# Kernel tuning notes

Hardware: AMD Instinct MI355X
Metric: run time of the kernel (lower is better)

Reference implementation:

```python
import jax, jax.numpy as jnp
import numpy as np

HEADS = 4
DIM_HEAD = 32
GN_EPS = 1e-6  # flax GroupNorm default


def setup_inputs() -> dict:
    key = jax.random.key(0)
    ks = jax.random.split(key, 3)
    B, H, W, C = 32, 64, 64, 256
    hidden = HEADS * DIM_HEAD  # 128
    x = jax.random.normal(ks[0], (B, H, W, C), dtype=jnp.float32)
    w_qkv = jax.random.normal(ks[1], (C, 3 * hidden), dtype=jnp.float32) * 0.02
    w_out = jax.random.normal(ks[2], (hidden, C), dtype=jnp.float32) * 0.02
    b_out = jnp.zeros((C,), dtype=jnp.float32)
    gn_scale = jnp.ones((C,), dtype=jnp.float32)
    gn_bias = jnp.zeros((C,), dtype=jnp.float32)
    return {"x": x, "w_qkv": w_qkv, "w_out": w_out, "b_out": b_out,
            "gn_scale": gn_scale, "gn_bias": gn_bias}


def reference(x, w_qkv, w_out, b_out, gn_scale, gn_bias):
    # x: [B, H, W, C] (flax Conv is channel-last)
    scale = DIM_HEAD ** (-0.5)
    qkv = jnp.einsum('bhwc,cd->bhwd', x, w_qkv)          # 1x1 conv, no bias
    q, k, v = jnp.split(qkv, 3, axis=-1)                 # each [B, H, W, hidden]
    q = jax.nn.softmax(q, axis=-2) * scale               # softmax over W axis
    k = jax.nn.softmax(k, axis=-1)                       # softmax over hidden axis
    # einsum axes as in source: b d n h / b e n h -> b d e h (d,e = H; n = W; h = hidden)
    context = jnp.einsum('bdnh,benh->bdeh', k, v)        # [B, H, H, hidden]
    out = jnp.einsum('bdeh,bdnh->benh', context, q)      # [B, H, W, hidden]
    y = jnp.einsum('bhwc,cd->bhwd', out, w_out) + b_out  # 1x1 conv with bias
    # GroupNorm(num_groups=1): normalize over (H, W, C) per sample
    mean = jnp.mean(y, axis=(1, 2, 3), keepdims=True)
    var = jnp.var(y, axis=(1, 2, 3), keepdims=True)
    y = (y - mean) * jax.lax.rsqrt(var + GN_EPS)
    return y * gn_scale + gn_bias
```

## Files before the change

kernel.cpp:

```cpp
#include <hip/hip_runtime.h>
#include <hip/hip_bf16.h>

typedef __hip_bfloat16 bf16;
typedef float f32x4 __attribute__((ext_vector_type(4)));
typedef short bf16x8 __attribute__((ext_vector_type(8)));
typedef short s16x4 __attribute__((ext_vector_type(4)));

#define NB 32
#define NC 256
#define NHID 128
#define NQKV 384
#define SMSCALE 0.17677669529663687f
#define PADA 264

__device__ __forceinline__ short f2bf(float f) {
  union { float f; unsigned u; } v;
  v.f = f;
  return (short)((v.u + 0x7fffu + ((v.u >> 16) & 1u)) >> 16);
}
__device__ __forceinline__ float bf2f(short s) {
  union { unsigned u; float f; } v;
  v.u = ((unsigned)(unsigned short)s) << 16;
  return v.f;
}

__global__ __launch_bounds__(256) void k_prep_w(const float* __restrict__ wqkv,
                                                const float* __restrict__ wout,
                                                short* __restrict__ wqt,
                                                short* __restrict__ wot) {
  int i = blockIdx.x * 256 + threadIdx.x;
  if (i < 98304) {
    int e = i & 7, l = (i >> 3) & 63, f = i >> 9;
    int nj = f % 6, g = f / 6;
    int ks = g & 7, s = g >> 3;
    int n = s * 96 + nj * 16 + (l & 15);
    int k = ks * 32 + (l >> 4) * 8 + e;
    wqt[i] = f2bf(wqkv[(size_t)k * NQKV + n]);
  }
  if (i < 32768) {
    int e = i & 7, l = (i >> 3) & 63, f = i >> 9;
    int nj = f & 3, g = f >> 2;
    int ks = g & 3, w = g >> 2;
    int c = w * 64 + nj * 16 + (l & 15);
    int k = ks * 32 + (l >> 4) * 8 + e;
    wot[i] = f2bf(wout[(size_t)k * NC + c]);
  }
}

__global__ __launch_bounds__(512) void k_gemm_qkv(const float* __restrict__ x,
                                                  const short* __restrict__ wqt,
                                                  short* __restrict__ qt,
                                                  short* __restrict__ kt,
                                                  short* __restrict__ vt) {
  __shared__ short As[64 * PADA];
  float* Ks = (float*)As;

  const int t = threadIdx.x;
  const int lane = t & 63;
  const int w = t >> 6;
  const int l15 = lane & 15;
  const int q = lane >> 4;
  const int h = w >> 2;
  const int strip = (w & 3) * 96;
  const int rowBase = blockIdx.x * 64;
  const int b = rowBase >> 12;
  const int d = (rowBase >> 6) & 63;

  {
    const int r = w;
    const int c = (t & 63) * 4;
#pragma unroll
    for (int it = 0; it < 8; ++it) {
      int row = it * 8 + r;
      float4 f = *(const float4*)(x + (size_t)(rowBase + row) * NC + c);
      s16x4 sv;
      sv[0] = f2bf(f.x); sv[1] = f2bf(f.y); sv[2] = f2bf(f.z); sv[3] = f2bf(f.w);
      *(s16x4*)(As + row * PADA + c) = sv;
    }
  }
  __syncthreads();

  const short* wqb = wqt + (((size_t)(w & 3) * 8) * 6) * 512 + lane * 8;

  f32x4 acc[2][6] = {};
  for (int ks = 0; ks < 8; ++ks) {
    const int k0 = ks * 32 + q * 8;
    bf16x8 afr[2];
#pragma unroll
    for (int mi = 0; mi < 2; ++mi)
      afr[mi] = *(const bf16x8*)(As + (h * 32 + mi * 16 + l15) * PADA + k0);
#pragma unroll
    for (int nj = 0; nj < 6; ++nj) {
      bf16x8 bfr = *(const bf16x8*)(wqb + (ks * 6 + nj) * 512);
#pragma unroll
      for (int mi = 0; mi < 2; ++mi)
        acc[mi][nj] = __builtin_amdgcn_mfma_f32_16x16x32_bf16(afr[mi], bfr, acc[mi][nj], 0, 0, 0);
    }
  }
  __syncthreads();

#pragma unroll
  for (int mi = 0; mi < 2; ++mi) {
#pragma unroll
    for (int nj = 0; nj < 6; ++nj) {
      const int g = strip + nj * 16 + l15;
      const int n_sp = h * 32 + mi * 16 + q * 4;
      if (g < 128) {
        s16x4 sv;
        sv[0] = f2bf(acc[mi][nj][0]); sv[1] = f2bf(acc[mi][nj][1]);
        sv[2] = f2bf(acc[mi][nj][2]); sv[3] = f2bf(acc[mi][nj][3]);
        *(s16x4*)(qt + (((size_t)(b * 128 + g)) << 12) + (d << 6) + n_sp) = sv;
      } else if (g < 256) {
        const int kc = g - 128;
#pragma unroll
        for (int rg = 0; rg < 4; ++rg)
          Ks[(n_sp + rg) * 132 + kc] = acc[mi][nj][rg];
      } else {
        s16x4 sv;
        sv[0] = f2bf(acc[mi][nj][0]); sv[1] = f2bf(acc[mi][nj][1]);
        sv[2] = f2bf(acc[mi][nj][2]); sv[3] = f2bf(acc[mi][nj][3]);
        *(s16x4*)(vt + (((size_t)(b * 128 + (g - 256))) << 12) + (d << 6) + n_sp) = sv;
      }
    }
  }
  __syncthreads();

  {
    const int r = t >> 3;
    const int c0 = (t & 7) * 16;
    float vals[16];
    float m = -1e30f;
#pragma unroll
    for (int i = 0; i < 16; ++i) {
      vals[i] = Ks[r * 132 + c0 + i];
      m = fmaxf(m, vals[i]);
    }
    m = fmaxf(m, __shfl_xor(m, 1, 64));
    m = fmaxf(m, __shfl_xor(m, 2, 64));
    m = fmaxf(m, __shfl_xor(m, 4, 64));
    float s = 0.f;
#pragma unroll
    for (int i = 0; i < 16; ++i) {
      vals[i] = __expf(vals[i] - m);
      s += vals[i];
    }
    s += __shfl_xor(s, 1, 64);
    s += __shfl_xor(s, 2, 64);
    s += __shfl_xor(s, 4, 64);
    const float rinv = 1.f / s;
#pragma unroll
    for (int i = 0; i < 16; ++i)
      Ks[r * 132 + c0 + i] = vals[i] * rinv;
  }
  __syncthreads();

  {
    const int n = t & 63;
    const int c0 = (t >> 6) * 16;
    const size_t obase = (((size_t)(b * 128)) << 12) + (d << 6) + n;
#pragma unroll
    for (int i = 0; i < 16; ++i)
      kt[obase + (((size_t)(c0 + i)) << 12)] = f2bf(Ks[n * 132 + c0 + i]);
  }
}

__global__ __launch_bounds__(256) void k_attn(const short* __restrict__ kt,
                                              const short* __restrict__ vt,
                                              const short* __restrict__ qt,
                                              short* __restrict__ at) {
  __shared__ short SK[4096];
  __shared__ short SV[4096];
  __shared__ short SC[4096];
  __shared__ short SP[4096];
  const int ch = blockIdx.x;
  const int b = blockIdx.y;
  const int t = threadIdx.x;
  const int lane = t & 63;
  const int w = t >> 6;
  const int l15 = lane & 15;
  const int q = lane >> 4;
  const size_t base = ((size_t)(b * 128 + ch)) << 12;

  {
    const int row = t >> 2;
    const int u0 = (t & 3) * 2;
    const int src = row * 64 + u0 * 8;
    bf16x8 k0 = *(const bf16x8*)(kt + base + src);
    bf16x8 k1 = *(const bf16x8*)(kt + base + src + 8);
    bf16x8 v0 = *(const bf16x8*)(vt + base + src);
    bf16x8 v1 = *(const bf16x8*)(vt + base + src + 8);
    const int r7 = row & 7;
    *(bf16x8*)(SK + row * 64 + ((u0 ^ r7) << 3)) = k0;
    *(bf16x8*)(SK + row * 64 + (((u0 + 1) ^ r7) << 3)) = k1;
    *(bf16x8*)(SV + row * 64 + ((u0 ^ r7) << 3)) = v0;
    *(bf16x8*)(SV + row * 64 + (((u0 + 1) ^ r7) << 3)) = v1;
  }
  {
    const int dd = t >> 2;
    const int c0 = (t & 3) * 16;
    bf16x8 q0 = *(const bf16x8*)(qt + base + dd * 64 + c0);
    bf16x8 q1 = *(const bf16x8*)(qt + base + dd * 64 + c0 + 8);
    float vals[16];
#pragma unroll
    for (int i = 0; i < 8; ++i) { vals[i] = bf2f(q0[i]); vals[8 + i] = bf2f(q1[i]); }
    float m = -1e30f;
#pragma unroll
    for (int i = 0; i < 16; ++i) m = fmaxf(m, vals[i]);
    m = fmaxf(m, __shfl_xor(m, 1, 64));
    m = fmaxf(m, __shfl_xor(m, 2, 64));
    float s = 0.f;
#pragma unroll
    for (int i = 0; i < 16; ++i) {
      vals[i] = __expf(vals[i] - m);
      s += vals[i];
    }
    s += __shfl_xor(s, 1, 64);
    s += __shfl_xor(s, 2, 64);
    const float r = SMSCALE / s;
    const int du = dd >> 3, doff = dd & 7;
#pragma unroll
    for (int i = 0; i < 16; ++i) {
      const int n = c0 + i;
      SP[n * 64 + ((du ^ (n & 7)) << 3) + doff] = f2bf(vals[i] * r);
    }
  }
  __syncthreads();

  f32x4 acc[4] = {};
#pragma unroll
  for (int ks = 0; ks < 2; ++ks) {
    const int rA = w * 16 + l15;
    bf16x8 afr = *(const bf16x8*)(SK + rA * 64 + (((ks * 4 + q) ^ (rA & 7)) << 3));
#pragma unroll
    for (int nj = 0; nj < 4; ++nj) {
      const int rB = nj * 16 + l15;
      bf16x8 bfr = *(const bf16x8*)(SV + rB * 64 + (((ks * 4 + q) ^ (rB & 7)) << 3));
      acc[nj] = __builtin_amdgcn_mfma_f32_16x16x32_bf16(afr, bfr, acc[nj], 0, 0, 0);
    }
  }
#pragma unroll
  for (int nj = 0; nj < 4; ++nj) {
    const int e = nj * 16 + l15;
    const int d0 = w * 16 + q * 4;
    s16x4 sv;
    sv[0] = f2bf(acc[nj][0]); sv[1] = f2bf(acc[nj][1]);
    sv[2] = f2bf(acc[nj][2]); sv[3] = f2bf(acc[nj][3]);
    *(s16x4*)(SC + e * 64 + (((d0 >> 3) ^ (e & 7)) << 3) + (d0 & 7)) = sv;
  }
  __syncthreads();

  f32x4 acc2[4] = {};
#pragma unroll
  for (int ks = 0; ks < 2; ++ks) {
    const int rA = w * 16 + l15;
    bf16x8 afr = *(const bf16x8*)(SP + rA * 64 + (((ks * 4 + q) ^ (rA & 7)) << 3));
#pragma unroll
    for (int nj = 0; nj < 4; ++nj) {
      const int rB = nj * 16 + l15;
      bf16x8 bfr = *(const bf16x8*)(SC + rB * 64 + (((ks * 4 + q) ^ (rB & 7)) << 3));
      acc2[nj] = __builtin_amdgcn_mfma_f32_16x16x32_bf16(afr, bfr, acc2[nj], 0, 0, 0);
    }
  }
#pragma unroll
  for (int nj = 0; nj < 4; ++nj) {
    const int e = nj * 16 + l15;
    const int n0 = w * 16 + q * 4;
    s16x4 sv;
    sv[0] = f2bf(acc2[nj][0]); sv[1] = f2bf(acc2[nj][1]);
    sv[2] = f2bf(acc2[nj][2]); sv[3] = f2bf(acc2[nj][3]);
    *(s16x4*)(at + base + e * 64 + n0) = sv;
  }
}

__global__ __launch_bounds__(256) void k_gemm_out(const short* __restrict__ at,
                                                  const short* __restrict__ wot,
                                                  const float* __restrict__ bias,
                                                  float* __restrict__ y,
                                                  float* __restrict__ sums) {
  __shared__ short As[64 * 128];
  __shared__ float red[8];
  const int t = threadIdx.x;
  const int lane = t & 63;
  const int w = t >> 6;
  const int l15 = lane & 15;
  const int q = lane >> 4;
  const int rowBase = blockIdx.x * 64;
  const int b = rowBase >> 12;
  const int r0 = rowBase & 4095;
  const size_t abase = (((size_t)(b * 128)) << 12) + r0;
  {
    const int tr = t & 15;
    const int tk = t >> 4;
#pragma unroll
    for (int i = 0; i < 2; ++i) {
      const int kq = tk + 16 * i;
      s16x4 f[4];
#pragma unroll
      for (int kc = 0; kc < 4; ++kc)
        f[kc] = *(const s16x4*)(at + abase + (((size_t)(kq * 4 + kc)) << 12) + tr * 4);
      const int ul = kq >> 1, hh = kq & 1;
#pragma unroll
      for (int j = 0; j < 4; ++j) {
        int m = tr * 4 + j;
        s16x4 sv;
        sv[0] = f[0][j]; sv[1] = f[1][j]; sv[2] = f[2][j]; sv[3] = f[3][j];
        *(s16x4*)(As + m * 128 + ((ul ^ (m & 15)) << 3) + hh * 4) = sv;
      }
    }
  }
  __syncthreads();
  const short* wob = wot + ((size_t)(w * 4) * 4) * 512 + lane * 8;
  f32x4 acc[4][4] = {};
  for (int ks = 0; ks < 4; ++ks) {
    bf16x8 afr[4];
#pragma unroll
    for (int mi = 0; mi < 4; ++mi) {
      int m = mi * 16 + l15;
      int ul = ks * 4 + q;
      afr[mi] = *(const bf16x8*)(As + m * 128 + ((ul ^ (m & 15)) << 3));
    }
#pragma unroll
    for (int nj = 0; nj < 4; ++nj) {
      bf16x8 bfr = *(const bf16x8*)(wob + (ks * 4 + nj) * 512);
#pragma unroll
      for (int mi = 0; mi < 4; ++mi)
        acc[mi][nj] = __builtin_amdgcn_mfma_f32_16x16x32_bf16(afr[mi], bfr, acc[mi][nj], 0, 0, 0);
    }
  }
  float ls = 0.f, lss = 0.f;
#pragma unroll
  for (int mi = 0; mi < 4; ++mi) {
    int r = rowBase + mi * 16 + q * 4;
#pragma unroll
    for (int nj = 0; nj < 4; ++nj) {
      int c = w * 64 + nj * 16 + l15;
      float bv = bias[c];
#pragma unroll
      for (int rg = 0; rg < 4; ++rg) {
        float v = acc[mi][nj][rg] + bv;
        y[(size_t)(r + rg) * NC + c] = v;
        ls += v;
        lss += v * v;
      }
    }
  }
#pragma unroll
  for (int off = 32; off; off >>= 1) {
    ls += __shfl_xor(ls, off, 64);
    lss += __shfl_xor(lss, off, 64);
  }
  if (lane == 0) {
    red[w] = ls;
    red[4 + w] = lss;
  }
  __syncthreads();
  if (t == 0) {
    float S = red[0] + red[1] + red[2] + red[3];
    float SS = red[4] + red[5] + red[6] + red[7];
    atomicAdd(&sums[2 * b], S);
    atomicAdd(&sums[2 * b + 1], SS);
  }
}

__global__ __launch_bounds__(256) void k_gnorm(float* __restrict__ y,
                                               const float* __restrict__ sums,
                                               const float* __restrict__ gs,
                                               const float* __restrict__ gb) {
  size_t i0 = ((size_t)blockIdx.x * 256 + threadIdx.x) * 4;
  int b = (int)(i0 >> 20);
  int c = (int)(i0 & 255);
  const float invN = 1.0f / 1048576.0f;
  float mean = sums[2 * b] * invN;
  float var = sums[2 * b + 1] * invN - mean * mean;
  float inv = rsqrtf(var + 1e-6f);
  float4 v = *((const float4*)(y + i0));
  float4 g = *((const float4*)(gs + c));
  float4 bb = *((const float4*)(gb + c));
  float4 r;
  r.x = (v.x - mean) * inv * g.x + bb.x;
  r.y = (v.y - mean) * inv * g.y + bb.y;
  r.z = (v.z - mean) * inv * g.z + bb.z;
  r.w = (v.w - mean) * inv * g.w + bb.w;
  *((float4*)(y + i0)) = r;
}

extern "C" void kernel_launch(void* const* d_in, const int* in_sizes, int n_in,
                              void* d_out, int out_size, void* d_ws, size_t ws_size,
                              hipStream_t stream) {
  const float* x = (const float*)d_in[0];
  const float* w_qkv = (const float*)d_in[1];
  const float* w_out = (const float*)d_in[2];
  const float* b_out = (const float*)d_in[3];
  const float* gn_scale = (const float*)d_in[4];
  const float* gn_bias = (const float*)d_in[5];
  float* out = (float*)d_out;

  char* ws = (char*)d_ws;
  const size_t SLAB = (size_t)67108864;
  short* qt = (short*)ws;
  short* kt = (short*)(ws + SLAB);
  short* vt = (short*)(ws + 2 * SLAB);
  short* at = qt;
  float* sums = (float*)(ws + 3 * SLAB);
  short* wqt = (short*)(ws + 3 * SLAB + 1024);
  short* wot = (short*)(ws + 3 * SLAB + 1024 + 196608);

  hipMemsetAsync(sums, 0, 64 * sizeof(float), stream);

  k_prep_w<<<384, 256, 0, stream>>>(w_qkv, w_out, wqt, wot);
  k_gemm_qkv<<<2048, 512, 0, stream>>>(x, wqt, qt, kt, vt);
  k_attn<<<dim3(128, 32), 256, 0, stream>>>(kt, vt, qt, at);
  k_gemm_out<<<2048, 256, 0, stream>>>(at, wot, b_out, out, sums);
  k_gnorm<<<32768, 256, 0, stream>>>(out, sums, gn_scale, gn_bias);
}
```

Measured before the change: 379.5 us.

## Store pre-norm output as bf16, one wave per attention channel, occupancy hint on QKV GEMM

The out-projection now stages its results through LDS and writes a bf16 intermediate instead of fp32. The GroupNorm kernel then reads that bf16 buffer and writes fp32 to the final output, roughly halving intermediate traffic. The attention kernel is restructured so each wave handles a whole channel independently: K/V fragments load straight from global memory into registers, the softmax is done per lane, and block-wide barriers are dropped. The QKV GEMM also gets a min-blocks launch bound. This trades precision in the pre-norm values and adds register pressure in attention (32 accumulator tiles per wave).

```diff
diff --git a/kernel.cpp b/kernel.cpp
--- a/kernel.cpp
+++ b/kernel.cpp
@@ -47,11 +47,11 @@
   }
 }
 
-__global__ __launch_bounds__(512) void k_gemm_qkv(const float* __restrict__ x,
-                                                  const short* __restrict__ wqt,
-                                                  short* __restrict__ qt,
-                                                  short* __restrict__ kt,
-                                                  short* __restrict__ vt) {
+__global__ __launch_bounds__(512, 6) void k_gemm_qkv(const float* __restrict__ x,
+                                                     const short* __restrict__ wqt,
+                                                     short* __restrict__ qt,
+                                                     short* __restrict__ kt,
+                                                     short* __restrict__ vt) {
   __shared__ short As[64 * PADA];
   float* Ks = (float*)As;
 
@@ -168,116 +168,110 @@
                                               const short* __restrict__ vt,
                                               const short* __restrict__ qt,
                                               short* __restrict__ at) {
-  __shared__ short SK[4096];
-  __shared__ short SV[4096];
-  __shared__ short SC[4096];
-  __shared__ short SP[4096];
-  const int ch = blockIdx.x;
-  const int b = blockIdx.y;
+  __shared__ short SP[4][4096];
+  __shared__ short SC[4][4096];
   const int t = threadIdx.x;
   const int lane = t & 63;
   const int w = t >> 6;
   const int l15 = lane & 15;
   const int q = lane >> 4;
+  const int ch = blockIdx.x * 4 + w;
+  const int b = blockIdx.y;
   const size_t base = ((size_t)(b * 128 + ch)) << 12;
+  short* sp = SP[w];
+  short* sc = SC[w];
 
   {
-    const int row = t >> 2;
-    const int u0 = (t & 3) * 2;
-    const int src = row * 64 + u0 * 8;
-    bf16x8 k0 = *(const bf16x8*)(kt + base + src);
-    bf16x8 k1 = *(const bf16x8*)(kt + base + src + 8);
-    bf16x8 v0 = *(const bf16x8*)(vt + base + src);
-    bf16x8 v1 = *(const bf16x8*)(vt + base + src + 8);
-    const int r7 = row & 7;
-    *(bf16x8*)(SK + row * 64 + ((u0 ^ r7) << 3)) = k0;
-    *(bf16x8*)(SK + row * 64 + (((u0 + 1) ^ r7) << 3)) = k1;
-    *(bf16x8*)(SV + row * 64 + ((u0 ^ r7) << 3)) = v0;
-    *(bf16x8*)(SV + row * 64 + (((u0 + 1) ^ r7) << 3)) = v1;
-  }
-  {
-    const int dd = t >> 2;
-    const int c0 = (t & 3) * 16;
-    bf16x8 q0 = *(const bf16x8*)(qt + base + dd * 64 + c0);
-    bf16x8 q1 = *(const bf16x8*)(qt + base + dd * 64 + c0 + 8);
-    float vals[16];
-#pragma unroll
-    for (int i = 0; i < 8; ++i) { vals[i] = bf2f(q0[i]); vals[8 + i] = bf2f(q1[i]); }
+    const short* qp = qt + base + lane * 64;
+    bf16x8 qr[8];
+#pragma unroll
+    for (int u = 0; u < 8; ++u) qr[u] = *(const bf16x8*)(qp + u * 8);
+    float vals[64];
     float m = -1e30f;
 #pragma unroll
-    for (int i = 0; i < 16; ++i) m = fmaxf(m, vals[i]);
-    m = fmaxf(m, __shfl_xor(m, 1, 64));
-    m = fmaxf(m, __shfl_xor(m, 2, 64));
+    for (int u = 0; u < 8; ++u)
+#pragma unroll
+      for (int i = 0; i < 8; ++i) {
+        float f = bf2f(qr[u][i]);
+        vals[u * 8 + i] = f;
+        m = fmaxf(m, f);
+      }
     float s = 0.f;
 #pragma unroll
-    for (int i = 0; i < 16; ++i) {
+    for (int i = 0; i < 64; ++i) {
       vals[i] = __expf(vals[i] - m);
       s += vals[i];
     }
-    s += __shfl_xor(s, 1, 64);
-    s += __shfl_xor(s, 2, 64);
     const float r = SMSCALE / s;
-    const int du = dd >> 3, doff = dd & 7;
-#pragma unroll
-    for (int i = 0; i < 16; ++i) {
-      const int n = c0 + i;
-      SP[n * 64 + ((du ^ (n & 7)) << 3) + doff] = f2bf(vals[i] * r);
-    }
-  }
-  __syncthreads();
-
-  f32x4 acc[4] = {};
+    const int du = lane >> 3, dof = lane & 7;
+#pragma unroll
+    for (int n = 0; n < 64; ++n)
+      sp[n * 64 + ((du ^ (n & 7)) << 3) + dof] = f2bf(vals[n] * r);
+  }
+
+  f32x4 acc1[4][4] = {};
 #pragma unroll
   for (int ks = 0; ks < 2; ++ks) {
-    const int rA = w * 16 + l15;
-    bf16x8 afr = *(const bf16x8*)(SK + rA * 64 + (((ks * 4 + q) ^ (rA & 7)) << 3));
-#pragma unroll
-    for (int nj = 0; nj < 4; ++nj) {
-      const int rB = nj * 16 + l15;
-      bf16x8 bfr = *(const bf16x8*)(SV + rB * 64 + (((ks * 4 + q) ^ (rB & 7)) << 3));
-      acc[nj] = __builtin_amdgcn_mfma_f32_16x16x32_bf16(afr, bfr, acc[nj], 0, 0, 0);
-    }
-  }
-#pragma unroll
-  for (int nj = 0; nj < 4; ++nj) {
-    const int e = nj * 16 + l15;
-    const int d0 = w * 16 + q * 4;
-    s16x4 sv;
-    sv[0] = f2bf(acc[nj][0]); sv[1] = f2bf(acc[nj][1]);
-    sv[2] = f2bf(acc[nj][2]); sv[3] = f2bf(acc[nj][3]);
-    *(s16x4*)(SC + e * 64 + (((d0 >> 3) ^ (e & 7)) << 3) + (d0 & 7)) = sv;
-  }
-  __syncthreads();
-
-  f32x4 acc2[4] = {};
+    bf16x8 kfr[4], vfr[4];
+#pragma unroll
+    for (int i = 0; i < 4; ++i) {
+      kfr[i] = *(const bf16x8*)(kt + base + (i * 16 + l15) * 64 + ks * 32 + q * 8);
+      vfr[i] = *(const bf16x8*)(vt + base + (i * 16 + l15) * 64 + ks * 32 + q * 8);
+    }
+#pragma unroll
+    for (int ds = 0; ds < 4; ++ds)
+#pragma unroll
+      for (int es = 0; es < 4; ++es)
+        acc1[ds][es] = __builtin_amdgcn_mfma_f32_16x16x32_bf16(kfr[ds], vfr[es], acc1[ds][es], 0, 0, 0);
+  }
+#pragma unroll
+  for (int ds = 0; ds < 4; ++ds)
+#pragma unroll
+    for (int es = 0; es < 4; ++es) {
+      const int e = es * 16 + l15;
+      const int d0 = ds * 16 + q * 4;
+      s16x4 sv;
+      sv[0] = f2bf(acc1[ds][es][0]); sv[1] = f2bf(acc1[ds][es][1]);
+      sv[2] = f2bf(acc1[ds][es][2]); sv[3] = f2bf(acc1[ds][es][3]);
+      *(s16x4*)(sc + e * 64 + (((d0 >> 3) ^ (e & 7)) << 3) + (d0 & 7)) = sv;
+    }
+
+  f32x4 acc2[4][4] = {};
 #pragma unroll
   for (int ks = 0; ks < 2; ++ks) {
-    const int rA = w * 16 + l15;
-    bf16x8 afr = *(const bf16x8*)(SP + rA * 64 + (((ks * 4 + q) ^ (rA & 7)) << 3));
-#pragma unroll
-    for (int nj = 0; nj < 4; ++nj) {
-      const int rB = nj * 16 + l15;
-      bf16x8 bfr = *(const bf16x8*)(SC + rB * 64 + (((ks * 4 + q) ^ (rB & 7)) << 3));
-      acc2[nj] = __builtin_amdgcn_mfma_f32_16x16x32_bf16(afr, bfr, acc2[nj], 0, 0, 0);
-    }
-  }
-#pragma unroll
-  for (int nj = 0; nj < 4; ++nj) {
-    const int e = nj * 16 + l15;
-    const int n0 = w * 16 + q * 4;
-    s16x4 sv;
-    sv[0] = f2bf(acc2[nj][0]); sv[1] = f2bf(acc2[nj][1]);
-    sv[2] = f2bf(acc2[nj][2]); sv[3] = f2bf(acc2[nj][3]);
-    *(s16x4*)(at + base + e * 64 + n0) = sv;
-  }
+    bf16x8 pfr[4], cfr[4];
+#pragma unroll
+    for (int i = 0; i < 4; ++i) {
+      const int rn = i * 16 + l15;
+      const int u = ((ks * 4 + q) ^ (rn & 7)) << 3;
+      pfr[i] = *(const bf16x8*)(sp + rn * 64 + u);
+      cfr[i] = *(const bf16x8*)(sc + rn * 64 + u);
+    }
+#pragma unroll
+    for (int na = 0; na < 4; ++na)
+#pragma unroll
+      for (int eb = 0; eb < 4; ++eb)
+        acc2[na][eb] = __builtin_amdgcn_mfma_f32_16x16x32_bf16(pfr[na], cfr[eb], acc2[na][eb], 0, 0, 0);
+  }
+#pragma unroll
+  for (int na = 0; na < 4; ++na)
+#pragma unroll
+    for (int eb = 0; eb < 4; ++eb) {
+      const int e = eb * 16 + l15;
+      const int n0 = na * 16 + q * 4;
+      s16x4 sv;
+      sv[0] = f2bf(acc2[na][eb][0]); sv[1] = f2bf(acc2[na][eb][1]);
+      sv[2] = f2bf(acc2[na][eb][2]); sv[3] = f2bf(acc2[na][eb][3]);
+      *(s16x4*)(at + base + e * 64 + n0) = sv;
+    }
 }
 
 __global__ __launch_bounds__(256) void k_gemm_out(const short* __restrict__ at,
                                                   const short* __restrict__ wot,
                                                   const float* __restrict__ bias,
-                                                  float* __restrict__ y,
+                                                  short* __restrict__ yb,
                                                   float* __restrict__ sums) {
-  __shared__ short As[64 * 128];
+  __shared__ short As[8448];
   __shared__ float red[8];
   const int t = threadIdx.x;
   const int lane = t & 63;
@@ -329,19 +323,32 @@
   }
   float ls = 0.f, lss = 0.f;
 #pragma unroll
-  for (int mi = 0; mi < 4; ++mi) {
-    int r = rowBase + mi * 16 + q * 4;
-#pragma unroll
-    for (int nj = 0; nj < 4; ++nj) {
-      int c = w * 64 + nj * 16 + l15;
-      float bv = bias[c];
-#pragma unroll
-      for (int rg = 0; rg < 4; ++rg) {
-        float v = acc[mi][nj][rg] + bv;
-        y[(size_t)(r + rg) * NC + c] = v;
-        ls += v;
-        lss += v * v;
+  for (int hh = 0; hh < 2; ++hh) {
+    __syncthreads();
+#pragma unroll
+    for (int mi2 = 0; mi2 < 2; ++mi2) {
+      const int mi = hh * 2 + mi2;
+#pragma unroll
+      for (int nj = 0; nj < 4; ++nj) {
+        const int c = w * 64 + nj * 16 + l15;
+        const float bv = bias[c];
+#pragma unroll
+        for (int rg = 0; rg < 4; ++rg) {
+          float v = acc[mi][nj][rg] + bv;
+          ls += v;
+          lss += v * v;
+          As[(mi2 * 16 + q * 4 + rg) * 264 + c] = f2bf(v);
+        }
       }
+    }
+    __syncthreads();
+    {
+      const int r = t >> 3;
+      const int c0 = (t & 7) * 32;
+      const size_t orow = (size_t)(rowBase + hh * 32 + r) * NC + c0;
+#pragma unroll
+      for (int u = 0; u < 4; ++u)
+        *(bf16x8*)(yb + orow + u * 8) = *(const bf16x8*)(As + r * 264 + c0 + u * 8);
     }
   }
 #pragma unroll
@@ -362,26 +369,34 @@
   }
 }
 
-__global__ __launch_bounds__(256) void k_gnorm(float* __restrict__ y,
+__global__ __launch_bounds__(256) void k_gnorm(const short* __restrict__ yb,
+                                               float* __restrict__ out,
                                                const float* __restrict__ sums,
                                                const float* __restrict__ gs,
                                                const float* __restrict__ gb) {
-  size_t i0 = ((size_t)blockIdx.x * 256 + threadIdx.x) * 4;
+  size_t i0 = ((size_t)blockIdx.x * 256 + threadIdx.x) * 8;
   int b = (int)(i0 >> 20);
   int c = (int)(i0 & 255);
   const float invN = 1.0f / 1048576.0f;
   float mean = sums[2 * b] * invN;
   float var = sums[2 * b + 1] * invN - mean * mean;
   float inv = rsqrtf(var + 1e-6f);
-  float4 v = *((const float4*)(y + i0));
-  float4 g = *((const float4*)(gs + c));
-  float4 bb = *((const float4*)(gb + c));
-  float4 r;
-  r.x = (v.x - mean) * inv * g.x + bb.x;
-  r.y = (v.y - mean) * inv * g.y + bb.y;
-  r.z = (v.z - mean) * inv * g.z + bb.z;
-  r.w = (v.w - mean) * inv * g.w + bb.w;
-  *((float4*)(y + i0)) = r;
+  bf16x8 v = *(const bf16x8*)(yb + i0);
+  float4 g0 = *(const float4*)(gs + c);
+  float4 g1 = *(const float4*)(gs + c + 4);
+  float4 b0 = *(const float4*)(gb + c);
+  float4 b1 = *(const float4*)(gb + c + 4);
+  float4 r0, r1;
+  r0.x = (bf2f(v[0]) - mean) * inv * g0.x + b0.x;
+  r0.y = (bf2f(v[1]) - mean) * inv * g0.y + b0.y;
+  r0.z = (bf2f(v[2]) - mean) * inv * g0.z + b0.z;
+  r0.w = (bf2f(v[3]) - mean) * inv * g0.w + b0.w;
+  r1.x = (bf2f(v[4]) - mean) * inv * g1.x + b1.x;
+  r1.y = (bf2f(v[5]) - mean) * inv * g1.y + b1.y;
+  r1.z = (bf2f(v[6]) - mean) * inv * g1.z + b1.z;
+  r1.w = (bf2f(v[7]) - mean) * inv * g1.w + b1.w;
+  *((float4*)(out + i0)) = r0;
+  *((float4*)(out + i0 + 4)) = r1;
 }
 
 extern "C" void kernel_launch(void* const* d_in, const int* in_sizes, int n_in,
@@ -401,6 +416,7 @@
   short* kt = (short*)(ws + SLAB);
   short* vt = (short*)(ws + 2 * SLAB);
   short* at = qt;
+  short* yb = kt;
   float* sums = (float*)(ws + 3 * SLAB);
   short* wqt = (short*)(ws + 3 * SLAB + 1024);
   short* wot = (short*)(ws + 3 * SLAB + 1024 + 196608);
@@ -409,7 +425,7 @@
 
   k_prep_w<<<384, 256, 0, stream>>>(w_qkv, w_out, wqt, wot);
   k_gemm_qkv<<<2048, 512, 0, stream>>>(x, wqt, qt, kt, vt);
-  k_attn<<<dim3(128, 32), 256, 0, stream>>>(kt, vt, qt, at);
-  k_gemm_out<<<2048, 256, 0, stream>>>(at, wot, b_out, out, sums);
-  k_gnorm<<<32768, 256, 0, stream>>>(out, sums, gn_scale, gn_bias);
-}
+  k_attn<<<dim3(32, 32), 256, 0, stream>>>(kt, vt, qt, at);
+  k_gemm_out<<<2048, 256, 0, stream>>>(at, wot, b_out, yb, sums);
+  k_gnorm<<<16384, 256, 0, stream>>>(yb, out, sums, gn_scale, gn_bias);
+}
```

After: 388.1 us. 2.3% more time.
